# Kernel optimization log

Measured on AMD Instinct MI355X. Metric: run time of the kernel, lower is better.

## Reference

```python
import jax, jax.numpy as jnp
import numpy as np

D_MODEL, D_K, D_V, H = 512, 64, 64, 8
B, NQ, NK = 2, 4096, 4096


def setup_inputs() -> dict:
    key = jax.random.key(0)
    ks = jax.random.split(key, 11)
    def xavier(k, shape):
        fan_in, fan_out = shape[1], shape[0]
        lim = jnp.sqrt(6.0 / (fan_in + fan_out))
        return jax.random.uniform(k, shape, jnp.float32, -lim, lim)
    return {
        "queries": jax.random.normal(ks[0], (B, NQ, D_MODEL), jnp.float32),
        "keys": jax.random.normal(ks[1], (B, NK, D_MODEL), jnp.float32),
        "values": jax.random.normal(ks[2], (B, NK, D_MODEL), jnp.float32),
        "Wq": xavier(ks[3], (H * D_K, D_MODEL)),
        "bq": jnp.zeros((H * D_K,), jnp.float32),
        "Wk": xavier(ks[4], (H * D_K, D_MODEL)),
        "bk": jnp.zeros((H * D_K,), jnp.float32),
        "Wv": xavier(ks[5], (H * D_V, D_MODEL)),
        "bv": jnp.zeros((H * D_V,), jnp.float32),
        "Wo": xavier(ks[6], (D_MODEL, H * D_V)),
        "bo": jnp.zeros((D_MODEL,), jnp.float32),
    }


def reference(queries, keys, values, Wq, bq, Wk, bk, Wv, bv, Wo, bo):
    b_s, nq, _ = queries.shape
    nk = keys.shape[1]
    # QKV projections (torch Linear: x @ W.T + b)
    q = (queries @ Wq.T + bq).reshape(b_s, nq, H, D_K).transpose(0, 2, 1, 3)  # b h nq dk
    k = (keys @ Wk.T + bk).reshape(b_s, nk, H, D_K).transpose(0, 2, 1, 3)     # b h nk dk
    v = (values @ Wv.T + bv).reshape(b_s, nk, H, D_V).transpose(0, 2, 1, 3)   # b h nk dv
    att = jnp.einsum("bhqd,bhkd->bhqk", q, k) / jnp.sqrt(jnp.float32(D_K))
    att = jax.nn.softmax(att, axis=-1)
    # dropout is identity in eval mode
    out = jnp.einsum("bhqk,bhkd->bhqd", att, v)
    out = out.transpose(0, 2, 1, 3).reshape(b_s, nq, H * D_V)
    return out @ Wo.T + bo
```

## Files before the change

### kernel.cpp

```cpp
#include <hip/hip_runtime.h>
#include <hip/hip_bf16.h>


typedef __attribute__((ext_vector_type(8))) short bf16x8;
typedef __attribute__((ext_vector_type(4))) float f32x4;
typedef __attribute__((ext_vector_type(16))) float f32x16;
typedef __attribute__((ext_vector_type(2))) int int2v;

#define SEQ  4096
#define DM   512
#define FPAD 72
#define VPAD 136
#define QSCALE 0.18033688011112042f
#define FSHIFT 16.0f

__device__ inline float fast_exp2(float x) {
#if __has_builtin(__builtin_amdgcn_exp2f)
    return __builtin_amdgcn_exp2f(x);
#else
    return __expf(x * 0.69314718056f);
#endif
}

__device__ inline unsigned pk2(float x, float y) {
#if __has_builtin(__builtin_amdgcn_cvt_pk_bf16_f32)
    typedef __attribute__((ext_vector_type(2))) __bf16 bf16x2_t;
    bf16x2_t h = __builtin_amdgcn_cvt_pk_bf16_f32(x, y);
    return *(unsigned*)&h;
#else
    unsigned ux = __float_as_uint(x);
    unsigned uy = __float_as_uint(y);
    ux += 0x7fff + ((ux >> 16) & 1);
    uy += 0x7fff + ((uy >> 16) & 1);
    return (ux >> 16) | (uy & 0xffff0000u);
#endif
}

__device__ inline int2v swap_half(unsigned a, unsigned b, int h) {
#if __has_builtin(__builtin_amdgcn_permlane32_swap)
    (void)h;
    return __builtin_amdgcn_permlane32_swap((int)a, (int)b, false, false);
#else
    unsigned ax = (unsigned)__shfl_xor((int)a, 32);
    unsigned bx = (unsigned)__shfl_xor((int)b, 32);
    int2v r;
    r.x = h ? (int)bx : (int)a;
    r.y = h ? (int)b  : (int)ax;
    return r;
#endif
}

__global__ __launch_bounds__(256) void cvt_w(
    const float* __restrict__ w0, const float* __restrict__ w1,
    const float* __restrict__ w2, const float* __restrict__ w3,
    __hip_bfloat16* __restrict__ o0, __hip_bfloat16* __restrict__ o1,
    __hip_bfloat16* __restrict__ o2, __hip_bfloat16* __restrict__ o3)
{
    const float* w = (blockIdx.y == 0) ? w0 : (blockIdx.y == 1) ? w1
                   : (blockIdx.y == 2) ? w2 : w3;
    __hip_bfloat16* o = (blockIdx.y == 0) ? o0 : (blockIdx.y == 1) ? o1
                      : (blockIdx.y == 2) ? o2 : o3;
    const int i = (blockIdx.x * 256 + threadIdx.x) * 4;
    float4 v = *(const float4*)&w[i];
    uint2 p;
    p.x = pk2(v.x, v.y);
    p.y = pk2(v.z, v.w);
    *(uint2*)&((unsigned short*)o)[i] = p;
}

__global__ __launch_bounds__(256) void qkv_proj(
    const float* __restrict__ Xq, const float* __restrict__ Xk, const float* __restrict__ Xv,
    const __hip_bfloat16* __restrict__ Wq16, const __hip_bfloat16* __restrict__ Wk16,
    const __hip_bfloat16* __restrict__ Wv16,
    const float* __restrict__ bq, const float* __restrict__ bk, const float* __restrict__ bv,
    __hip_bfloat16* __restrict__ Oq, __hip_bfloat16* __restrict__ Ok,
    __hip_bfloat16* __restrict__ Ovt)
{
    const int z = blockIdx.z;
    const float* A          = (z == 0) ? Xq : (z == 1) ? Xk : Xv;
    const __hip_bfloat16* W = (z == 0) ? Wq16 : (z == 1) ? Wk16 : Wv16;
    const float* bias       = (z == 0) ? bq : (z == 1) ? bk : bv;

    __shared__ __align__(16) short As[64 * 32];
    __shared__ __align__(16) short Ws2[128 * 32];

    const int bm   = blockIdx.x * 64;
    const int bn   = blockIdx.y * 128;
    const int tid  = threadIdx.x;
    const int wave = tid >> 6;
    const int lane = tid & 63;
    const int quad = lane >> 4;
    const int l16  = lane & 15;

    const int srow = tid >> 2;
    const int scol = (tid & 3) * 8;

    f32x4 acc[8] = {};

    float4 a0 = *(const float4*)&A[(size_t)(bm + srow) * DM + scol];
    float4 a1 = *(const float4*)&A[(size_t)(bm + srow) * DM + scol + 4];
    bf16x8 w0 = *(const bf16x8*)&W[(size_t)(bn + srow) * DM + scol];
    bf16x8 w1 = *(const bf16x8*)&W[(size_t)(bn + srow + 64) * DM + scol];

    for (int k0 = 0; k0 < DM; k0 += 32) {
        uint4 pa = {pk2(a0.x, a0.y), pk2(a0.z, a0.w), pk2(a1.x, a1.y), pk2(a1.z, a1.w)};

        __syncthreads();
        *(uint4*)&As[srow * 32 + scol] = pa;
        *(bf16x8*)&Ws2[srow * 32 + scol] = w0;
        *(bf16x8*)&Ws2[(srow + 64) * 32 + scol] = w1;
        __syncthreads();

        if (k0 + 32 < DM) {
            a0 = *(const float4*)&A[(size_t)(bm + srow) * DM + k0 + 32 + scol];
            a1 = *(const float4*)&A[(size_t)(bm + srow) * DM + k0 + 32 + scol + 4];
            w0 = *(const bf16x8*)&W[(size_t)(bn + srow) * DM + k0 + 32 + scol];
            w1 = *(const bf16x8*)&W[(size_t)(bn + srow + 64) * DM + k0 + 32 + scol];
        }

        bf16x8 a = *(bf16x8*)&As[(wave * 16 + l16) * 32 + quad * 8];
#pragma unroll
        for (int nt = 0; nt < 8; nt++) {
            bf16x8 b = *(bf16x8*)&Ws2[(nt * 16 + l16) * 32 + quad * 8];
            acc[nt] = __builtin_amdgcn_mfma_f32_16x16x32_bf16(a, b, acc[nt], 0, 0, 0);
        }
    }

    if (z == 2) {
        const int row0 = bm + wave * 16 + quad * 4;
        const int b    = row0 >> 12;
        const int seq0 = row0 & 4095;
        unsigned short* Vt = (unsigned short*)Ovt;
#pragma unroll
        for (int nt = 0; nt < 8; nt++) {
            const int col = bn + nt * 16 + l16;
            const float bv_ = bias[col];
            uint2 pk;
            pk.x = pk2(acc[nt][0] + bv_, acc[nt][1] + bv_);
            pk.y = pk2(acc[nt][2] + bv_, acc[nt][3] + bv_);
            *(uint2*)&Vt[((size_t)(b * 512 + col)) * 4096 + seq0] = pk;
        }
    } else {
        unsigned short* C = (unsigned short*)((z == 0) ? Oq : Ok);
        const float scale = (z == 0) ? QSCALE : 1.0f;
        const size_t row0 = bm + wave * 16 + quad * 4;
#pragma unroll
        for (int nt = 0; nt < 8; nt++) {
            const int col = bn + nt * 16 + l16;
            const float bv_ = bias[col];
            unsigned u01 = pk2((acc[nt][0] + bv_) * scale, (acc[nt][1] + bv_) * scale);
            unsigned u23 = pk2((acc[nt][2] + bv_) * scale, (acc[nt][3] + bv_) * scale);
            C[(row0 + 0) * DM + col] = (unsigned short)(u01 & 0xffff);
            C[(row0 + 1) * DM + col] = (unsigned short)(u01 >> 16);
            C[(row0 + 2) * DM + col] = (unsigned short)(u23 & 0xffff);
            C[(row0 + 3) * DM + col] = (unsigned short)(u23 >> 16);
        }
    }
}

__global__ __launch_bounds__(512, 4) void flash_attn(
    const __hip_bfloat16* __restrict__ Q,
    const __hip_bfloat16* __restrict__ K,
    const __hip_bfloat16* __restrict__ Vt,
    __hip_bfloat16* __restrict__ O)
{
    __shared__ __align__(16) short Ks[128 * FPAD];
    __shared__ __align__(16) short Vs[64 * VPAD];

    const int q0  = blockIdx.x * 128;
    const int bh  = blockIdx.y;
    const int tid = threadIdx.x;
    const int wave = tid >> 6;
    const int lane = tid & 63;
    const int L = lane & 31;
    const int h = lane >> 5;
    const int qg  = wave & 3;
    const int kvg = wave >> 2;

    const __hip_bfloat16* Qb = Q + (size_t)(bh >> 3) * SEQ * DM + (bh & 7) * 64;
    const __hip_bfloat16* Kb = K + (size_t)(bh >> 3) * SEQ * DM + (bh & 7) * 64;
    const __hip_bfloat16* Vb = Vt + (size_t)bh * 64 * SEQ;
    __hip_bfloat16*       Ob = O + (size_t)(bh >> 3) * SEQ * DM + (bh & 7) * 64;

    const int kr = tid >> 3;
    const int kc = (tid & 7) * 8;
    const int vr = tid >> 4;
    const int vc = (tid & 15) * 8;

    const int qrow = q0 + qg * 32 + L;
    bf16x8 bq[4];
#pragma unroll
    for (int db = 0; db < 4; db++)
        bq[db] = *(const bf16x8*)&Qb[(size_t)qrow * DM + db * 16 + h * 8];

    const __hip_bfloat16* kg = Kb + (size_t)kr * DM + kc;
    const __hip_bfloat16* vg = Vb + (size_t)vr * SEQ + vc;

    bf16x8 kp[2], vp[2];
    kp[0] = *(const bf16x8*)(kg);
    kp[1] = *(const bf16x8*)(kg + (size_t)64 * DM);
    vp[0] = *(const bf16x8*)(vg);
    vp[1] = *(const bf16x8*)(vg + (size_t)32 * SEQ);

    const short* ksb = &Ks[L * FPAD + h * 8];
    const short* vsb = &Vs[L * VPAD + h * 8];

    f32x16 oacc[2] = {};
    float l0 = 0.0f, l1 = 0.0f;

    for (int kv0 = 0; kv0 < SEQ; kv0 += 128) {
        __syncthreads();
        *(bf16x8*)&Ks[kr * FPAD + kc] = kp[0];
        *(bf16x8*)&Ks[(kr + 64) * FPAD + kc] = kp[1];
        *(bf16x8*)&Vs[vr * VPAD + vc] = vp[0];
        *(bf16x8*)&Vs[(vr + 32) * VPAD + vc] = vp[1];
        __syncthreads();

        kg += (size_t)128 * DM;
        vg += 128;
        if (kv0 + 128 < SEQ) {
            kp[0] = *(const bf16x8*)(kg);
            kp[1] = *(const bf16x8*)(kg + (size_t)64 * DM);
            vp[0] = *(const bf16x8*)(vg);
            vp[1] = *(const bf16x8*)(vg + (size_t)32 * SEQ);
        }

#pragma unroll
        for (int kb2 = 0; kb2 < 2; kb2++) {
            const int kb = kvg * 2 + kb2;
            f32x16 s;
#pragma unroll
            for (int r = 0; r < 16; r++) s[r] = -FSHIFT;
            __builtin_amdgcn_s_setprio(1);
#pragma unroll
            for (int db = 0; db < 4; db++) {
                bf16x8 ak = *(const bf16x8*)&ksb[(kb * 32) * FPAD + db * 16];
                s = __builtin_amdgcn_mfma_f32_32x32x16_bf16(ak, bq[db], s, 0, 0, 0);
            }
            __builtin_amdgcn_s_setprio(0);

#pragma unroll
            for (int r = 0; r < 16; r++) s[r] = fast_exp2(s[r]);

#pragma unroll
            for (int r = 0; r < 16; r += 2) { l0 += s[r]; l1 += s[r + 1]; }

            unsigned pk_[8];
#pragma unroll
            for (int j = 0; j < 8; j++) pk_[j] = pk2(s[2 * j], s[2 * j + 1]);

            int2v w0 = swap_half(pk_[0], pk_[2], h);
            int2v w1 = swap_half(pk_[1], pk_[3], h);
            int2v w2 = swap_half(pk_[4], pk_[6], h);
            int2v w3 = swap_half(pk_[5], pk_[7], h);
            uint4 f0u = {(unsigned)w0.x, (unsigned)w1.x, (unsigned)w0.y, (unsigned)w1.y};
            uint4 f1u = {(unsigned)w2.x, (unsigned)w3.x, (unsigned)w2.y, (unsigned)w3.y};
            bf16x8 fg0 = *(bf16x8*)&f0u;
            bf16x8 fg1 = *(bf16x8*)&f1u;

            __builtin_amdgcn_s_setprio(1);
#pragma unroll
            for (int dvb = 0; dvb < 2; dvb++) {
                bf16x8 av0 = *(const bf16x8*)&vsb[(dvb * 32) * VPAD + kb * 32];
                bf16x8 av1 = *(const bf16x8*)&vsb[(dvb * 32) * VPAD + kb * 32 + 16];
                oacc[dvb] = __builtin_amdgcn_mfma_f32_32x32x16_bf16(av0, fg0, oacc[dvb], 0, 0, 0);
                oacc[dvb] = __builtin_amdgcn_mfma_f32_32x32x16_bf16(av1, fg1, oacc[dvb], 0, 0, 0);
            }
            __builtin_amdgcn_s_setprio(0);
        }
    }

    float lsum = l0 + l1;
    float tot = lsum + __shfl_xor(lsum, 32);

    __syncthreads();
    float* area = (qg < 2) ? (float*)Ks : (float*)Vs;
    float* slot = area + (qg & 1) * (64 * 33) + lane * 33;
    if (kvg == 1) {
#pragma unroll
        for (int dvb = 0; dvb < 2; dvb++)
#pragma unroll
            for (int r = 0; r < 16; r++) slot[dvb * 16 + r] = oacc[dvb][r];
        slot[32] = tot;
    }
    __syncthreads();
    if (kvg == 0) {
#pragma unroll
        for (int dvb = 0; dvb < 2; dvb++)
#pragma unroll
            for (int r = 0; r < 16; r++) oacc[dvb][r] += slot[dvb * 16 + r];
        tot += slot[32];

        const float inv = 1.0f / tot;
        unsigned short* Op = (unsigned short*)Ob;
#pragma unroll
        for (int dvb = 0; dvb < 2; dvb++)
#pragma unroll
            for (int b = 0; b < 4; b++) {
                uint2 ov;
                ov.x = pk2(oacc[dvb][4 * b + 0] * inv, oacc[dvb][4 * b + 1] * inv);
                ov.y = pk2(oacc[dvb][4 * b + 2] * inv, oacc[dvb][4 * b + 3] * inv);
                *(uint2*)&Op[(size_t)qrow * DM + dvb * 32 + b * 8 + h * 4] = ov;
            }
    }
}

__global__ __launch_bounds__(256) void out_proj(
    const __hip_bfloat16* __restrict__ A,
    const __hip_bfloat16* __restrict__ W,
    const float* __restrict__ bias,
    float* __restrict__ C)
{
    __shared__ __align__(16) short As[64 * 32];
    __shared__ __align__(16) short Ws2[128 * 32];

    const int bm   = blockIdx.x * 64;
    const int bn   = blockIdx.y * 128;
    const int tid  = threadIdx.x;
    const int wave = tid >> 6;
    const int lane = tid & 63;
    const int quad = lane >> 4;
    const int l16  = lane & 15;

    const int srow = tid >> 2;
    const int scol = (tid & 3) * 8;

    f32x4 acc[8] = {};

    bf16x8 ap = *(const bf16x8*)&A[(size_t)(bm + srow) * DM + scol];
    bf16x8 w0 = *(const bf16x8*)&W[(size_t)(bn + srow) * DM + scol];
    bf16x8 w1 = *(const bf16x8*)&W[(size_t)(bn + srow + 64) * DM + scol];

    for (int k0 = 0; k0 < DM; k0 += 32) {
        __syncthreads();
        *(bf16x8*)&As[srow * 32 + scol] = ap;
        *(bf16x8*)&Ws2[srow * 32 + scol] = w0;
        *(bf16x8*)&Ws2[(srow + 64) * 32 + scol] = w1;
        __syncthreads();

        if (k0 + 32 < DM) {
            ap = *(const bf16x8*)&A[(size_t)(bm + srow) * DM + k0 + 32 + scol];
            w0 = *(const bf16x8*)&W[(size_t)(bn + srow) * DM + k0 + 32 + scol];
            w1 = *(const bf16x8*)&W[(size_t)(bn + srow + 64) * DM + k0 + 32 + scol];
        }

        bf16x8 a = *(bf16x8*)&As[(wave * 16 + l16) * 32 + quad * 8];
#pragma unroll
        for (int nt = 0; nt < 8; nt++) {
            bf16x8 b = *(bf16x8*)&Ws2[(nt * 16 + l16) * 32 + quad * 8];
            acc[nt] = __builtin_amdgcn_mfma_f32_16x16x32_bf16(a, b, acc[nt], 0, 0, 0);
        }
    }

#pragma unroll
    for (int nt = 0; nt < 8; nt++) {
        const int col = bn + nt * 16 + l16;
        const float bv_ = bias[col];
#pragma unroll
        for (int r = 0; r < 4; r++) {
            const int row = bm + wave * 16 + quad * 4 + r;
            C[(size_t)row * DM + col] = acc[nt][r] + bv_;
        }
    }
}

extern "C" void kernel_launch(void* const* d_in, const int* in_sizes, int n_in,
                              void* d_out, int out_size, void* d_ws, size_t ws_size,
                              hipStream_t stream) {
    const float* queries = (const float*)d_in[0];
    const float* keys    = (const float*)d_in[1];
    const float* values  = (const float*)d_in[2];
    const float* Wq = (const float*)d_in[3];
    const float* bq = (const float*)d_in[4];
    const float* Wk = (const float*)d_in[5];
    const float* bk = (const float*)d_in[6];
    const float* Wv = (const float*)d_in[7];
    const float* bv = (const float*)d_in[8];
    const float* Wo = (const float*)d_in[9];
    const float* bo = (const float*)d_in[10];
    float* out = (float*)d_out;

    const size_t MS = (size_t)2 * SEQ * DM;
    const size_t WN = (size_t)DM * DM;
    __hip_bfloat16* q_ws  = (__hip_bfloat16*)d_ws;
    __hip_bfloat16* k_ws  = q_ws + MS;
    __hip_bfloat16* vt_ws = k_ws + MS;
    __hip_bfloat16* o_ws  = vt_ws + MS;
    __hip_bfloat16* wq16  = o_ws + MS;
    __hip_bfloat16* wk16  = wq16 + WN;
    __hip_bfloat16* wv16  = wk16 + WN;
    __hip_bfloat16* wo16  = wv16 + WN;

    dim3 blk(256);

    cvt_w<<<dim3(256, 4), blk, 0, stream>>>(Wq, Wk, Wv, Wo, wq16, wk16, wv16, wo16);

    qkv_proj<<<dim3(128, 4, 3), blk, 0, stream>>>(
        queries, keys, values, wq16, wk16, wv16, bq, bk, bv, q_ws, k_ws, vt_ws);

    flash_attn<<<dim3(32, 16), dim3(512), 0, stream>>>(q_ws, k_ws, vt_ws, o_ws);

    out_proj<<<dim3(128, 4), blk, 0, stream>>>(o_ws, wo16, bo, out);
}
```

Measured before the change: 236.2 us.

## Double-buffer K/V tiles in LDS to halve block barriers per tile

Splits the K and V shared-memory tiles into two buffers. While the block computes on one buffer, it writes the prefetched next tile into the other, so each KV tile needs one barrier instead of two. This doubles LDS use per block to roughly 72 KB, which may reduce how many 512-thread blocks fit on a CU compared with the launch-bounds target of four.

```diff
diff --git a/kernel.cpp b/kernel.cpp
--- a/kernel.cpp
+++ b/kernel.cpp
@@ -164,8 +164,8 @@
     const __hip_bfloat16* __restrict__ Vt,
     __hip_bfloat16* __restrict__ O)
 {
-    __shared__ __align__(16) short Ks[128 * FPAD];
-    __shared__ __align__(16) short Vs[64 * VPAD];
+    __shared__ __align__(16) short Ks[2][128 * FPAD];
+    __shared__ __align__(16) short Vs[2][64 * VPAD];
 
     const int q0  = blockIdx.x * 128;
     const int bh  = blockIdx.y;
@@ -197,34 +197,28 @@
     const __hip_bfloat16* vg = Vb + (size_t)vr * SEQ + vc;
 
     bf16x8 kp[2], vp[2];
-    kp[0] = *(const bf16x8*)(kg);
-    kp[1] = *(const bf16x8*)(kg + (size_t)64 * DM);
-    vp[0] = *(const bf16x8*)(vg);
-    vp[1] = *(const bf16x8*)(vg + (size_t)32 * SEQ);
-
-    const short* ksb = &Ks[L * FPAD + h * 8];
-    const short* vsb = &Vs[L * VPAD + h * 8];
+    auto load_regs = [&]() {
+        kp[0] = *(const bf16x8*)(kg);
+        kp[1] = *(const bf16x8*)(kg + (size_t)64 * DM);
+        vp[0] = *(const bf16x8*)(vg);
+        vp[1] = *(const bf16x8*)(vg + (size_t)32 * SEQ);
+        kg += (size_t)128 * DM;
+        vg += 128;
+    };
+    auto stage_write = [&](short* Kd, short* Vd) {
+        *(bf16x8*)&Kd[kr * FPAD + kc] = kp[0];
+        *(bf16x8*)&Kd[(kr + 64) * FPAD + kc] = kp[1];
+        *(bf16x8*)&Vd[vr * VPAD + vc] = vp[0];
+        *(bf16x8*)&Vd[(vr + 32) * VPAD + vc] = vp[1];
+    };
+
+    const short* ksbp[2] = { &Ks[0][L * FPAD + h * 8], &Ks[1][L * FPAD + h * 8] };
+    const short* vsbp[2] = { &Vs[0][L * VPAD + h * 8], &Vs[1][L * VPAD + h * 8] };
 
     f32x16 oacc[2] = {};
     float l0 = 0.0f, l1 = 0.0f;
 
-    for (int kv0 = 0; kv0 < SEQ; kv0 += 128) {
-        __syncthreads();
-        *(bf16x8*)&Ks[kr * FPAD + kc] = kp[0];
-        *(bf16x8*)&Ks[(kr + 64) * FPAD + kc] = kp[1];
-        *(bf16x8*)&Vs[vr * VPAD + vc] = vp[0];
-        *(bf16x8*)&Vs[(vr + 32) * VPAD + vc] = vp[1];
-        __syncthreads();
-
-        kg += (size_t)128 * DM;
-        vg += 128;
-        if (kv0 + 128 < SEQ) {
-            kp[0] = *(const bf16x8*)(kg);
-            kp[1] = *(const bf16x8*)(kg + (size_t)64 * DM);
-            vp[0] = *(const bf16x8*)(vg);
-            vp[1] = *(const bf16x8*)(vg + (size_t)32 * SEQ);
-        }
-
+    auto compute = [&](const short* ksb, const short* vsb) {
 #pragma unroll
         for (int kb2 = 0; kb2 < 2; kb2++) {
             const int kb = kvg * 2 + kb2;
@@ -268,6 +262,21 @@
             }
             __builtin_amdgcn_s_setprio(0);
         }
+    };
+
+    load_regs();
+    stage_write(&Ks[0][0], &Vs[0][0]);
+    load_regs();
+
+    for (int t = 0; t < 32; t += 2) {
+        __syncthreads();
+        compute(ksbp[0], vsbp[0]);
+        if (t + 1 < 32) stage_write(&Ks[1][0], &Vs[1][0]);
+        if (t + 2 < 32) load_regs();
+        __syncthreads();
+        compute(ksbp[1], vsbp[1]);
+        if (t + 2 < 32) stage_write(&Ks[0][0], &Vs[0][0]);
+        if (t + 3 < 32) load_regs();
     }
 
     float lsum = l0 + l1;
```

Measured after the change: 470.2 us. +99.0%, slower.

## Enlarge projection GEMM tiles to 128x128 with 32x32x16 MFMA and padded LDS

Applied to the files above, without the earlier changes.

Rewrites the QKV and output projection GEMMs to use 128x128 block tiles with a 64-wide K step. Each wave now computes a 64x64 sub-tile using four 32x32x16 bf16 MFMAs, and LDS rows are padded to 72 to avoid bank conflicts. The aim is more reuse of each LDS load per MFMA, fewer barriers per unit of K, and less global traffic per output. In exchange the grid is halved, which leaves fewer blocks to fill the GPU, and register pressure rises from the larger accumulators and prefetch buffers.

```diff
diff --git a/kernel.cpp b/kernel.cpp
--- a/kernel.cpp
+++ b/kernel.cpp
@@ -11,6 +11,7 @@
 #define DM   512
 #define FPAD 72
 #define VPAD 136
+#define GPAD 72
 #define QSCALE 0.18033688011112042f
 #define FSHIFT 16.0f
 
@@ -81,80 +82,120 @@
     const __hip_bfloat16* W = (z == 0) ? Wq16 : (z == 1) ? Wk16 : Wv16;
     const float* bias       = (z == 0) ? bq : (z == 1) ? bk : bv;
 
-    __shared__ __align__(16) short As[64 * 32];
-    __shared__ __align__(16) short Ws2[128 * 32];
-
-    const int bm   = blockIdx.x * 64;
+    __shared__ __align__(16) short As[128 * GPAD];
+    __shared__ __align__(16) short Ws2[128 * GPAD];
+
+    const int bm   = blockIdx.x * 128;
     const int bn   = blockIdx.y * 128;
     const int tid  = threadIdx.x;
     const int wave = tid >> 6;
     const int lane = tid & 63;
-    const int quad = lane >> 4;
-    const int l16  = lane & 15;
-
-    const int srow = tid >> 2;
-    const int scol = (tid & 3) * 8;
-
-    f32x4 acc[8] = {};
-
-    float4 a0 = *(const float4*)&A[(size_t)(bm + srow) * DM + scol];
-    float4 a1 = *(const float4*)&A[(size_t)(bm + srow) * DM + scol + 4];
-    bf16x8 w0 = *(const bf16x8*)&W[(size_t)(bn + srow) * DM + scol];
-    bf16x8 w1 = *(const bf16x8*)&W[(size_t)(bn + srow + 64) * DM + scol];
-
-    for (int k0 = 0; k0 < DM; k0 += 32) {
-        uint4 pa = {pk2(a0.x, a0.y), pk2(a0.z, a0.w), pk2(a1.x, a1.y), pk2(a1.z, a1.w)};
-
-        __syncthreads();
-        *(uint4*)&As[srow * 32 + scol] = pa;
-        *(bf16x8*)&Ws2[srow * 32 + scol] = w0;
-        *(bf16x8*)&Ws2[(srow + 64) * 32 + scol] = w1;
-        __syncthreads();
-
-        if (k0 + 32 < DM) {
-            a0 = *(const float4*)&A[(size_t)(bm + srow) * DM + k0 + 32 + scol];
-            a1 = *(const float4*)&A[(size_t)(bm + srow) * DM + k0 + 32 + scol + 4];
-            w0 = *(const bf16x8*)&W[(size_t)(bn + srow) * DM + k0 + 32 + scol];
-            w1 = *(const bf16x8*)&W[(size_t)(bn + srow + 64) * DM + k0 + 32 + scol];
-        }
-
-        bf16x8 a = *(bf16x8*)&As[(wave * 16 + l16) * 32 + quad * 8];
-#pragma unroll
-        for (int nt = 0; nt < 8; nt++) {
-            bf16x8 b = *(bf16x8*)&Ws2[(nt * 16 + l16) * 32 + quad * 8];
-            acc[nt] = __builtin_amdgcn_mfma_f32_16x16x32_bf16(a, b, acc[nt], 0, 0, 0);
+    const int L = lane & 31;
+    const int h = lane >> 5;
+    const int wr = wave >> 1;
+    const int wc = wave & 1;
+
+    const int srow = tid >> 1;
+    const int scl  = (tid & 1) * 32;
+
+    f32x16 acc[2][2] = {};
+
+    float4 av[8];
+    bf16x8 wv[4];
+#pragma unroll
+    for (int j = 0; j < 8; j++)
+        av[j] = *(const float4*)&A[(size_t)(bm + srow) * DM + scl + 4 * j];
+#pragma unroll
+    for (int j = 0; j < 4; j++)
+        wv[j] = *(const bf16x8*)&W[(size_t)(bn + srow) * DM + scl + 8 * j];
+
+    const short* asb = &As[(wr * 64 + L) * GPAD + h * 8];
+    const short* bsb = &Ws2[(wc * 64 + L) * GPAD + h * 8];
+
+    for (int k0 = 0; k0 < DM; k0 += 64) {
+        uint4 pa[4];
+#pragma unroll
+        for (int i = 0; i < 4; i++) {
+            pa[i].x = pk2(av[2 * i].x, av[2 * i].y);
+            pa[i].y = pk2(av[2 * i].z, av[2 * i].w);
+            pa[i].z = pk2(av[2 * i + 1].x, av[2 * i + 1].y);
+            pa[i].w = pk2(av[2 * i + 1].z, av[2 * i + 1].w);
+        }
+
+        __syncthreads();
+#pragma unroll
+        for (int i = 0; i < 4; i++)
+            *(uint4*)&As[srow * GPAD + scl + 8 * i] = pa[i];
+#pragma unroll
+        for (int j = 0; j < 4; j++)
+            *(bf16x8*)&Ws2[srow * GPAD + scl + 8 * j] = wv[j];
+        __syncthreads();
+
+        if (k0 + 64 < DM) {
+            const int k = k0 + 64;
+#pragma unroll
+            for (int j = 0; j < 8; j++)
+                av[j] = *(const float4*)&A[(size_t)(bm + srow) * DM + k + scl + 4 * j];
+#pragma unroll
+            for (int j = 0; j < 4; j++)
+                wv[j] = *(const bf16x8*)&W[(size_t)(bn + srow) * DM + k + scl + 8 * j];
+        }
+
+#pragma unroll
+        for (int ks = 0; ks < 4; ks++) {
+            bf16x8 a0 = *(const bf16x8*)&asb[ks * 16];
+            bf16x8 a1 = *(const bf16x8*)&asb[32 * GPAD + ks * 16];
+            bf16x8 b0 = *(const bf16x8*)&bsb[ks * 16];
+            bf16x8 b1 = *(const bf16x8*)&bsb[32 * GPAD + ks * 16];
+            acc[0][0] = __builtin_amdgcn_mfma_f32_32x32x16_bf16(a0, b0, acc[0][0], 0, 0, 0);
+            acc[0][1] = __builtin_amdgcn_mfma_f32_32x32x16_bf16(a0, b1, acc[0][1], 0, 0, 0);
+            acc[1][0] = __builtin_amdgcn_mfma_f32_32x32x16_bf16(a1, b0, acc[1][0], 0, 0, 0);
+            acc[1][1] = __builtin_amdgcn_mfma_f32_32x32x16_bf16(a1, b1, acc[1][1], 0, 0, 0);
         }
     }
 
     if (z == 2) {
-        const int row0 = bm + wave * 16 + quad * 4;
-        const int b    = row0 >> 12;
-        const int seq0 = row0 & 4095;
+        const int bnum = bm >> 12;
+        const int seqb = bm & 4095;
         unsigned short* Vt = (unsigned short*)Ovt;
 #pragma unroll
-        for (int nt = 0; nt < 8; nt++) {
-            const int col = bn + nt * 16 + l16;
-            const float bv_ = bias[col];
-            uint2 pk;
-            pk.x = pk2(acc[nt][0] + bv_, acc[nt][1] + bv_);
-            pk.y = pk2(acc[nt][2] + bv_, acc[nt][3] + bv_);
-            *(uint2*)&Vt[((size_t)(b * 512 + col)) * 4096 + seq0] = pk;
-        }
+        for (int mb = 0; mb < 2; mb++)
+#pragma unroll
+            for (int nb = 0; nb < 2; nb++) {
+                const int col = bn + wc * 64 + nb * 32 + L;
+                const float bv_ = bias[col];
+                unsigned short* vt = &Vt[((size_t)(bnum * 512 + col)) * 4096];
+#pragma unroll
+                for (int g = 0; g < 4; g++) {
+                    const int seq = seqb + wr * 64 + mb * 32 + 4 * h + 8 * g;
+                    uint2 ov;
+                    ov.x = pk2(acc[mb][nb][4 * g + 0] + bv_, acc[mb][nb][4 * g + 1] + bv_);
+                    ov.y = pk2(acc[mb][nb][4 * g + 2] + bv_, acc[mb][nb][4 * g + 3] + bv_);
+                    *(uint2*)&vt[seq] = ov;
+                }
+            }
     } else {
         unsigned short* C = (unsigned short*)((z == 0) ? Oq : Ok);
         const float scale = (z == 0) ? QSCALE : 1.0f;
-        const size_t row0 = bm + wave * 16 + quad * 4;
-#pragma unroll
-        for (int nt = 0; nt < 8; nt++) {
-            const int col = bn + nt * 16 + l16;
-            const float bv_ = bias[col];
-            unsigned u01 = pk2((acc[nt][0] + bv_) * scale, (acc[nt][1] + bv_) * scale);
-            unsigned u23 = pk2((acc[nt][2] + bv_) * scale, (acc[nt][3] + bv_) * scale);
-            C[(row0 + 0) * DM + col] = (unsigned short)(u01 & 0xffff);
-            C[(row0 + 1) * DM + col] = (unsigned short)(u01 >> 16);
-            C[(row0 + 2) * DM + col] = (unsigned short)(u23 & 0xffff);
-            C[(row0 + 3) * DM + col] = (unsigned short)(u23 >> 16);
-        }
+#pragma unroll
+        for (int mb = 0; mb < 2; mb++)
+#pragma unroll
+            for (int nb = 0; nb < 2; nb++) {
+                const int col = bn + wc * 64 + nb * 32 + L;
+                const float bv_ = bias[col];
+#pragma unroll
+                for (int g = 0; g < 4; g++) {
+                    const int row = bm + wr * 64 + mb * 32 + 4 * h + 8 * g;
+                    unsigned u01 = pk2((acc[mb][nb][4 * g + 0] + bv_) * scale,
+                                       (acc[mb][nb][4 * g + 1] + bv_) * scale);
+                    unsigned u23 = pk2((acc[mb][nb][4 * g + 2] + bv_) * scale,
+                                       (acc[mb][nb][4 * g + 3] + bv_) * scale);
+                    C[(size_t)(row + 0) * DM + col] = (unsigned short)(u01 & 0xffff);
+                    C[(size_t)(row + 1) * DM + col] = (unsigned short)(u01 >> 16);
+                    C[(size_t)(row + 2) * DM + col] = (unsigned short)(u23 & 0xffff);
+                    C[(size_t)(row + 3) * DM + col] = (unsigned short)(u23 >> 16);
+                }
+            }
     }
 }
 
@@ -311,57 +352,79 @@
     const float* __restrict__ bias,
     float* __restrict__ C)
 {
-    __shared__ __align__(16) short As[64 * 32];
-    __shared__ __align__(16) short Ws2[128 * 32];
-
-    const int bm   = blockIdx.x * 64;
+    __shared__ __align__(16) short As[128 * GPAD];
+    __shared__ __align__(16) short Ws2[128 * GPAD];
+
+    const int bm   = blockIdx.x * 128;
     const int bn   = blockIdx.y * 128;
     const int tid  = threadIdx.x;
     const int wave = tid >> 6;
     const int lane = tid & 63;
-    const int quad = lane >> 4;
-    const int l16  = lane & 15;
-
-    const int srow = tid >> 2;
-    const int scol = (tid & 3) * 8;
-
-    f32x4 acc[8] = {};
-
-    bf16x8 ap = *(const bf16x8*)&A[(size_t)(bm + srow) * DM + scol];
-    bf16x8 w0 = *(const bf16x8*)&W[(size_t)(bn + srow) * DM + scol];
-    bf16x8 w1 = *(const bf16x8*)&W[(size_t)(bn + srow + 64) * DM + scol];
-
-    for (int k0 = 0; k0 < DM; k0 += 32) {
-        __syncthreads();
-        *(bf16x8*)&As[srow * 32 + scol] = ap;
-        *(bf16x8*)&Ws2[srow * 32 + scol] = w0;
-        *(bf16x8*)&Ws2[(srow + 64) * 32 + scol] = w1;
-        __syncthreads();
-
-        if (k0 + 32 < DM) {
-            ap = *(const bf16x8*)&A[(size_t)(bm + srow) * DM + k0 + 32 + scol];
-            w0 = *(const bf16x8*)&W[(size_t)(bn + srow) * DM + k0 + 32 + scol];
-            w1 = *(const bf16x8*)&W[(size_t)(bn + srow + 64) * DM + k0 + 32 + scol];
-        }
-
-        bf16x8 a = *(bf16x8*)&As[(wave * 16 + l16) * 32 + quad * 8];
-#pragma unroll
-        for (int nt = 0; nt < 8; nt++) {
-            bf16x8 b = *(bf16x8*)&Ws2[(nt * 16 + l16) * 32 + quad * 8];
-            acc[nt] = __builtin_amdgcn_mfma_f32_16x16x32_bf16(a, b, acc[nt], 0, 0, 0);
-        }
-    }
-
-#pragma unroll
-    for (int nt = 0; nt < 8; nt++) {
-        const int col = bn + nt * 16 + l16;
-        const float bv_ = bias[col];
-#pragma unroll
-        for (int r = 0; r < 4; r++) {
-            const int row = bm + wave * 16 + quad * 4 + r;
-            C[(size_t)row * DM + col] = acc[nt][r] + bv_;
-        }
-    }
+    const int L = lane & 31;
+    const int h = lane >> 5;
+    const int wr = wave >> 1;
+    const int wc = wave & 1;
+
+    const int srow = tid >> 1;
+    const int scl  = (tid & 1) * 32;
+
+    f32x16 acc[2][2] = {};
+
+    bf16x8 avv[4], wv[4];
+#pragma unroll
+    for (int j = 0; j < 4; j++) {
+        avv[j] = *(const bf16x8*)&A[(size_t)(bm + srow) * DM + scl + 8 * j];
+        wv[j]  = *(const bf16x8*)&W[(size_t)(bn + srow) * DM + scl + 8 * j];
+    }
+
+    const short* asb = &As[(wr * 64 + L) * GPAD + h * 8];
+    const short* bsb = &Ws2[(wc * 64 + L) * GPAD + h * 8];
+
+    for (int k0 = 0; k0 < DM; k0 += 64) {
+        __syncthreads();
+#pragma unroll
+        for (int j = 0; j < 4; j++) {
+            *(bf16x8*)&As[srow * GPAD + scl + 8 * j] = avv[j];
+            *(bf16x8*)&Ws2[srow * GPAD + scl + 8 * j] = wv[j];
+        }
+        __syncthreads();
+
+        if (k0 + 64 < DM) {
+            const int k = k0 + 64;
+#pragma unroll
+            for (int j = 0; j < 4; j++) {
+                avv[j] = *(const bf16x8*)&A[(size_t)(bm + srow) * DM + k + scl + 8 * j];
+                wv[j]  = *(const bf16x8*)&W[(size_t)(bn + srow) * DM + k + scl + 8 * j];
+            }
+        }
+
+#pragma unroll
+        for (int ks = 0; ks < 4; ks++) {
+            bf16x8 a0 = *(const bf16x8*)&asb[ks * 16];
+            bf16x8 a1 = *(const bf16x8*)&asb[32 * GPAD + ks * 16];
+            bf16x8 b0 = *(const bf16x8*)&bsb[ks * 16];
+            bf16x8 b1 = *(const bf16x8*)&bsb[32 * GPAD + ks * 16];
+            acc[0][0] = __builtin_amdgcn_mfma_f32_32x32x16_bf16(a0, b0, acc[0][0], 0, 0, 0);
+            acc[0][1] = __builtin_amdgcn_mfma_f32_32x32x16_bf16(a0, b1, acc[0][1], 0, 0, 0);
+            acc[1][0] = __builtin_amdgcn_mfma_f32_32x32x16_bf16(a1, b0, acc[1][0], 0, 0, 0);
+            acc[1][1] = __builtin_amdgcn_mfma_f32_32x32x16_bf16(a1, b1, acc[1][1], 0, 0, 0);
+        }
+    }
+
+#pragma unroll
+    for (int mb = 0; mb < 2; mb++)
+#pragma unroll
+        for (int nb = 0; nb < 2; nb++) {
+            const int col = bn + wc * 64 + nb * 32 + L;
+            const float bv_ = bias[col];
+#pragma unroll
+            for (int g = 0; g < 4; g++) {
+                const int row = bm + wr * 64 + mb * 32 + 4 * h + 8 * g;
+#pragma unroll
+                for (int j = 0; j < 4; j++)
+                    C[(size_t)(row + j) * DM + col] = acc[mb][nb][4 * g + j] + bv_;
+            }
+        }
 }
 
 extern "C" void kernel_launch(void* const* d_in, const int* in_sizes, int n_in,
@@ -395,10 +458,10 @@
 
     cvt_w<<<dim3(256, 4), blk, 0, stream>>>(Wq, Wk, Wv, Wo, wq16, wk16, wv16, wo16);
 
-    qkv_proj<<<dim3(128, 4, 3), blk, 0, stream>>>(
+    qkv_proj<<<dim3(64, 4, 3), blk, 0, stream>>>(
         queries, keys, values, wq16, wk16, wv16, bq, bk, bv, q_ws, k_ws, vt_ws);
 
     flash_attn<<<dim3(32, 16), dim3(512), 0, stream>>>(q_ws, k_ws, vt_ws, o_ws);
 
-    out_proj<<<dim3(128, 4), blk, 0, stream>>>(o_ws, wo16, bo, out);
-}
+    out_proj<<<dim3(64, 4), blk, 0, stream>>>(o_ws, wo16, bo, out);
+}
```

Result: no change. 239.3 us (+1.3%).
